# Optimization experiments

Hardware: AMD Instinct MI355X
Metric: run time of the kernel (lower is better)

The kernel has to match this reference:

```python
import jax, jax.numpy as jnp
import numpy as np

# dims: batch N, queries Q, frames F, patches-per-frame L, heads H, head_dim D
N, Q, F, L, H, D = 32, 64, 16, 196, 12, 64
E = H * D          # embed_dim = 768
K = F * L          # kv length = 3136


def setup_inputs() -> dict:
    key = jax.random.key(0)
    kq, kk, kv, km, kw1, kw2 = jax.random.split(key, 6)
    q = jax.random.normal(kq, (N, Q, E), dtype=jnp.float32)
    k = jax.random.normal(kk, (N, K, H, D), dtype=jnp.float32)
    v = jax.random.normal(kv, (N, K, H, D), dtype=jnp.float32)
    # frame-padding mask; guarantee >=1 valid patch per frame so the
    # per-frame softmax never sees an all -inf group (NaN otherwise)
    m = jax.random.bernoulli(km, 0.9, (N, K))
    m = m.reshape(N, F, L).at[:, :, 0].set(True).reshape(N, K)
    W_in = jax.random.normal(kw1, (E, E), dtype=jnp.float32) * 0.02   # in_proj (n_act=1)
    W_out = jax.random.normal(kw2, (E, E), dtype=jnp.float32) * 0.02  # out_proj
    return {"q": q, "k": k, "v": v, "m": m, "W_in": W_in, "W_out": W_out}


def reference(q, k, v, m, W_in, W_out):
    n, nq, e = q.shape
    h, d = H, e // H
    # in_proj (no bias) then split into heads; n_act == 1 so qs has one element
    qs = (q @ W_in.T).reshape(n, nq, h, d)
    # scaled QK affinity: [n, Q, K, h]
    aff = jnp.einsum('nqhc,nkhc->nqkh', qs * (d ** -0.5), k)
    # frame mask broadcast over queries and heads
    aff = jnp.where(m[:, None, :, None], aff, -jnp.inf)
    kn = aff.shape[2]
    # grouped softmax over patches within each frame (dim=-2 of the view)
    aff = jax.nn.softmax(aff.reshape(n, nq, F, kn // F, h), axis=-2)
    aff = aff.reshape(n, nq, kn, h)
    # mix with v and output projection
    mix = jnp.einsum('nqlh,nlhc->nqhc', aff, v)
    out = mix.reshape(n, nq, e) @ W_out.T
    # second return: stacked flattened qs, shape [n, n_act=1, Q, E]
    qs_out = qs.reshape(n, nq, e)[:, None]
    return out, qs_out
```

## Files before the change

### kernel.cpp

```cpp
#include <hip/hip_runtime.h>
#include <hip/hip_bf16.h>
#include <cfloat>

#define N_B 32
#define QN 64
#define FN 16
#define LP 196
#define HN 12
#define DH 64
#define EE 768
#define KLEN 3136
#define FPB 4
#define KROWS 208
#define VST 256
#define PST 232

typedef short s16x4 __attribute__((ext_vector_type(4)));
typedef __bf16 bf16x8 __attribute__((ext_vector_type(8)));
typedef float f32x4 __attribute__((ext_vector_type(4)));

__device__ __forceinline__ bf16x8 cvt8(f32x4 a, f32x4 b) {
    bf16x8 r;
    r[0] = (__bf16)a[0]; r[1] = (__bf16)a[1]; r[2] = (__bf16)a[2]; r[3] = (__bf16)a[3];
    r[4] = (__bf16)b[0]; r[5] = (__bf16)b[1]; r[6] = (__bf16)b[2]; r[7] = (__bf16)b[3];
    return r;
}
__device__ __forceinline__ unsigned short bfb(float x) {
    return __builtin_bit_cast(unsigned short, (__bf16)x);
}

__global__ __launch_bounds__(256) void gemm_mfma(const float* __restrict__ A,
                                                 const float* __restrict__ W,
                                                 float* __restrict__ C) {
    __shared__ unsigned short As[64 * 72];
    __shared__ unsigned short Ws[48 * 72];
    const int t = threadIdx.x;
    const int w = t >> 6, lane = t & 63, lr = lane & 15, lg = lane >> 4;
    const int m0 = blockIdx.x * 64;
    const int n0 = blockIdx.y * 48;

    f32x4 acc[3];
#pragma unroll
    for (int ct = 0; ct < 3; ++ct) acc[ct] = (f32x4){0.f, 0.f, 0.f, 0.f};

    for (int k0 = 0; k0 < EE; k0 += 32) {
        {
            int row = t >> 2, cb = t & 3;
            const float* src = A + (size_t)(m0 + row) * EE + k0 + cb * 8;
            f32x4 a = *(const f32x4*)src, b = *(const f32x4*)(src + 4);
            *(bf16x8*)&As[row * 72 + cb * 8] = cvt8(a, b);
        }
        if (t < 192) {
            int row = t >> 2, cb = t & 3;
            const float* src = W + (size_t)(n0 + row) * EE + k0 + cb * 8;
            f32x4 a = *(const f32x4*)src, b = *(const f32x4*)(src + 4);
            *(bf16x8*)&Ws[row * 72 + cb * 8] = cvt8(a, b);
        }
        __syncthreads();
        bf16x8 a = *(const bf16x8*)&As[(w * 16 + lr) * 72 + lg * 8];
#pragma unroll
        for (int ct = 0; ct < 3; ++ct) {
            bf16x8 b = *(const bf16x8*)&Ws[(ct * 16 + lr) * 72 + lg * 8];
            acc[ct] = __builtin_amdgcn_mfma_f32_16x16x32_bf16(a, b, acc[ct], 0, 0, 0);
        }
        __syncthreads();
    }
#pragma unroll
    for (int ct = 0; ct < 3; ++ct)
#pragma unroll
        for (int r = 0; r < 4; ++r)
            C[(size_t)(m0 + w * 16 + lg * 4 + r) * EE + n0 + ct * 16 + lr] = acc[ct][r];
}

__global__ __launch_bounds__(256) void zero_f32(float* __restrict__ p, int n4) {
    int i = blockIdx.x * 256 + threadIdx.x;
    if (i < n4) ((float4*)p)[i] = make_float4(0.f, 0.f, 0.f, 0.f);
}

__global__ __launch_bounds__(256, 2) void attn_mfma(const float* __restrict__ qs_g,
                                                    const float* __restrict__ k_g,
                                                    const float* __restrict__ v_g,
                                                    const int* __restrict__ m_g,
                                                    float* __restrict__ mix_g) {
    const int h = blockIdx.x, fg = blockIdx.y, n = blockIdx.z;

    __shared__ unsigned short KV_s[64 * VST];
    __shared__ unsigned short Pt_s[64 * PST];
    __shared__ float bias_s[224];
    __shared__ float linv_s[4][16];

    const int t = threadIdx.x;
    const int w = t >> 6, lane = t & 63, lr = lane & 15, lg = lane >> 4;

    {
        int qr = t >> 2, c0 = 208 + (t & 3) * 4;
        *(s16x4*)&Pt_s[qr * PST + c0] = (s16x4){0, 0, 0, 0};
    }
    bf16x8 qb0, qb1;
    {
        const float* qp = qs_g + ((size_t)n * QN + w * 16 + lr) * EE + h * DH + lg * 8;
        f32x4 a = *(const f32x4*)qp, b = *(const f32x4*)(qp + 4);
        f32x4 c = *(const f32x4*)(qp + 32), d = *(const f32x4*)(qp + 36);
#pragma unroll
        for (int i = 0; i < 4; ++i) { a[i] *= 0.125f; b[i] *= 0.125f; c[i] *= 0.125f; d[i] *= 0.125f; }
        qb0 = cvt8(a, b);
        qb1 = cvt8(c, d);
    }

    float mix[4][4];
#pragma unroll
    for (int dt = 0; dt < 4; ++dt)
#pragma unroll
        for (int r = 0; r < 4; ++r) mix[dt][r] = 0.f;

    for (int ff = 0; ff < FPB; ++ff) {
        const size_t kbase = (size_t)n * KLEN + (size_t)(fg * FPB + ff) * LP;

        __syncthreads();

#pragma unroll
        for (int u = 0; u < 7; ++u) {
            int unit = t + 256 * u;
            if (unit < KROWS * 8) {
                int p = unit >> 3, blk = unit & 7;
                f32x4 a = {0.f, 0.f, 0.f, 0.f}, b = {0.f, 0.f, 0.f, 0.f};
                if (p < LP) {
                    const float* src = k_g + ((kbase + p) * HN + h) * DH + blk * 8;
                    a = *(const f32x4*)src;
                    b = *(const f32x4*)(src + 4);
                }
                *(bf16x8*)&KV_s[p * 64 + ((blk ^ (p & 7)) << 3)] = cvt8(a, b);
            }
        }
        if (t < 224) {
            float bv = -1e30f;
            if (t < LP && m_g[kbase + t] != 0) bv = 0.f;
            bias_s[t] = bv;
        }
        __syncthreads();

        f32x4 sc[13];
#pragma unroll
        for (int tl = 0; tl < 13; ++tl) {
            int row = tl * 16 + lr;
            bf16x8 a0 = *(const bf16x8*)&KV_s[row * 64 + ((lg ^ (lr & 7)) << 3)];
            bf16x8 a1 = *(const bf16x8*)&KV_s[row * 64 + (((4 + lg) ^ (lr & 7)) << 3)];
            f32x4 z = {0.f, 0.f, 0.f, 0.f};
            z = __builtin_amdgcn_mfma_f32_16x16x32_bf16(a0, qb0, z, 0, 0, 0);
            sc[tl] = __builtin_amdgcn_mfma_f32_16x16x32_bf16(a1, qb1, z, 0, 0, 0);
        }

        f32x4 va[7], vb[7];
#pragma unroll
        for (int u = 0; u < 7; ++u) {
            int unit = t + 256 * u;
            int pp = unit >> 4, d4 = unit & 15;
            int p0 = pp * 2;
            va[u] = (f32x4){0.f, 0.f, 0.f, 0.f};
            vb[u] = (f32x4){0.f, 0.f, 0.f, 0.f};
            if (p0 < LP) {
                const float* vg = v_g + ((kbase + p0) * HN + h) * DH + d4 * 4;
                va[u] = *(const f32x4*)vg;
                if (p0 + 1 < LP) vb[u] = *(const f32x4*)(vg + (size_t)HN * DH);
            }
        }

        float mx = -FLT_MAX;
#pragma unroll
        for (int tl = 0; tl < 13; ++tl)
#pragma unroll
            for (int r = 0; r < 4; ++r) {
                float sv = sc[tl][r] + bias_s[tl * 16 + lg * 4 + r];
                sc[tl][r] = sv;
                mx = fmaxf(mx, sv);
            }
        mx = fmaxf(mx, __shfl_xor(mx, 16));
        mx = fmaxf(mx, __shfl_xor(mx, 32));
        float sum = 0.f;
#pragma unroll
        for (int tl = 0; tl < 13; ++tl)
#pragma unroll
            for (int r = 0; r < 4; ++r) {
                float e = __expf(sc[tl][r] - mx);
                sc[tl][r] = e;
                sum += e;
            }
        sum += __shfl_xor(sum, 16);
        sum += __shfl_xor(sum, 32);
        if (lane < 16) linv_s[w][lane] = 1.0f / sum;

#pragma unroll
        for (int tl = 0; tl < 13; ++tl) {
            s16x4 pb = {(short)bfb(sc[tl][0]), (short)bfb(sc[tl][1]),
                        (short)bfb(sc[tl][2]), (short)bfb(sc[tl][3])};
            *(s16x4*)&Pt_s[(w * 16 + lr) * PST + tl * 16 + lg * 4] = pb;
        }
        __syncthreads();

#pragma unroll
        for (int u = 0; u < 7; ++u) {
            int unit = t + 256 * u;
            int pp = unit >> 4, d4 = unit & 15;
            int p0 = pp * 2;
            int blk = p0 >> 3, sub = p0 & 7;
#pragma unroll
            for (int i = 0; i < 4; ++i) {
                int row = d4 * 4 + i;
                int g = (row + (row >> 2)) & 7;
                unsigned pk = (unsigned)bfb(va[u][i]) | ((unsigned)bfb(vb[u][i]) << 16);
                *(unsigned*)&KV_s[row * VST + (((blk ^ g) << 3) | sub)] = pk;
            }
        }
        __syncthreads();

        f32x4 pv[4];
#pragma unroll
        for (int dt = 0; dt < 4; ++dt) pv[dt] = (f32x4){0.f, 0.f, 0.f, 0.f};
#pragma unroll
        for (int ks = 0; ks < 7; ++ks) {
            bf16x8 a = *(const bf16x8*)&Pt_s[(w * 16 + lr) * PST + ks * 32 + lg * 8];
#pragma unroll
            for (int dt = 0; dt < 4; ++dt) {
                int row = dt * 16 + lr;
                int g = (row + (row >> 2)) & 7;
                bf16x8 b = *(const bf16x8*)&KV_s[row * VST + (((ks * 4 + lg) ^ g) << 3)];
                pv[dt] = __builtin_amdgcn_mfma_f32_16x16x32_bf16(a, b, pv[dt], 0, 0, 0);
            }
        }
        float li[4];
#pragma unroll
        for (int r = 0; r < 4; ++r) li[r] = linv_s[w][lg * 4 + r];
#pragma unroll
        for (int dt = 0; dt < 4; ++dt)
#pragma unroll
            for (int r = 0; r < 4; ++r) mix[dt][r] += pv[dt][r] * li[r];
    }

#pragma unroll
    for (int dt = 0; dt < 4; ++dt)
#pragma unroll
        for (int r = 0; r < 4; ++r)
            atomicAdd(mix_g + ((size_t)n * QN + w * 16 + lg * 4 + r) * EE + h * DH + dt * 16 + lr,
                      mix[dt][r]);
}

extern "C" void kernel_launch(void* const* d_in, const int* in_sizes, int n_in,
                              void* d_out, int out_size, void* d_ws, size_t ws_size,
                              hipStream_t stream) {
    const float* q  = (const float*)d_in[0];
    const float* k  = (const float*)d_in[1];
    const float* v  = (const float*)d_in[2];
    const int*   m  = (const int*)d_in[3];
    const float* Wi = (const float*)d_in[4];
    const float* Wo = (const float*)d_in[5];

    float* out = (float*)d_out;
    float* qs  = out + (size_t)N_B * QN * EE;
    float* mix = (float*)d_ws;

    const int mix_n4 = (N_B * QN * EE) / 4;
    dim3 ggrid((N_B * QN) / 64, EE / 48);
    gemm_mfma<<<ggrid, 256, 0, stream>>>(q, Wi, qs);
    zero_f32<<<(mix_n4 + 255) / 256, 256, 0, stream>>>(mix, mix_n4);
    attn_mfma<<<dim3(HN, FN / FPB, N_B), 256, 0, stream>>>(qs, k, v, m, mix);
    gemm_mfma<<<ggrid, 256, 0, stream>>>(mix, Wo, out);
}
```

Measured before the change: 221.6 us.

## Keep softmax probabilities in registers via lane shuffles, drop Pt LDS buffer

Removes the shared-memory staging of the bf16 probability matrix and the linv buffer. Probabilities are packed in registers and rearranged into the MFMA A-operand layout with cross-lane shuffles, and the 1/sum values are broadcast with shuffles. The smaller LDS footprint allows raising launch bounds to 4 blocks per CU, and FPB drops from 4 to 2, doubling the grid and the atomic adds. The V swizzle pattern changes, V loads move after the softmax (less register prefetch overlap), and the extra shuffles add VALU/LDS-permute work.

```diff
diff --git a/kernel.cpp b/kernel.cpp
--- a/kernel.cpp
+++ b/kernel.cpp
@@ -10,14 +10,14 @@
 #define DH 64
 #define EE 768
 #define KLEN 3136
-#define FPB 4
+#define FPB 2
 #define KROWS 208
 #define VST 256
-#define PST 232
 
 typedef short s16x4 __attribute__((ext_vector_type(4)));
 typedef __bf16 bf16x8 __attribute__((ext_vector_type(8)));
 typedef float f32x4 __attribute__((ext_vector_type(4)));
+typedef unsigned u32x4 __attribute__((ext_vector_type(4)));
 
 __device__ __forceinline__ bf16x8 cvt8(f32x4 a, f32x4 b) {
     bf16x8 r;
@@ -27,6 +27,9 @@
 }
 __device__ __forceinline__ unsigned short bfb(float x) {
     return __builtin_bit_cast(unsigned short, (__bf16)x);
+}
+__device__ __forceinline__ unsigned pkbf(float lo, float hi) {
+    return (unsigned)bfb(lo) | ((unsigned)bfb(hi) << 16);
 }
 
 __global__ __launch_bounds__(256) void gemm_mfma(const float* __restrict__ A,
@@ -77,25 +80,19 @@
     if (i < n4) ((float4*)p)[i] = make_float4(0.f, 0.f, 0.f, 0.f);
 }
 
-__global__ __launch_bounds__(256, 2) void attn_mfma(const float* __restrict__ qs_g,
+__global__ __launch_bounds__(256, 4) void attn_mfma(const float* __restrict__ qs_g,
                                                     const float* __restrict__ k_g,
                                                     const float* __restrict__ v_g,
                                                     const int* __restrict__ m_g,
                                                     float* __restrict__ mix_g) {
     const int h = blockIdx.x, fg = blockIdx.y, n = blockIdx.z;
 
-    __shared__ unsigned short KV_s[64 * VST];
-    __shared__ unsigned short Pt_s[64 * PST];
-    __shared__ float bias_s[224];
-    __shared__ float linv_s[4][16];
+    __shared__ __attribute__((aligned(16))) unsigned short KV_s[64 * VST];
+    __shared__ __attribute__((aligned(16))) float bias_s[224];
 
     const int t = threadIdx.x;
     const int w = t >> 6, lane = t & 63, lr = lane & 15, lg = lane >> 4;
 
-    {
-        int qr = t >> 2, c0 = 208 + (t & 3) * 4;
-        *(s16x4*)&Pt_s[qr * PST + c0] = (s16x4){0, 0, 0, 0};
-    }
     bf16x8 qb0, qb1;
     {
         const float* qp = qs_g + ((size_t)n * QN + w * 16 + lr) * EE + h * DH + lg * 8;
@@ -150,65 +147,58 @@
             sc[tl] = __builtin_amdgcn_mfma_f32_16x16x32_bf16(a1, qb1, z, 0, 0, 0);
         }
 
-        f32x4 va[7], vb[7];
+        float mx = -FLT_MAX;
+#pragma unroll
+        for (int tl = 0; tl < 13; ++tl) {
+            f32x4 bv = *(const f32x4*)&bias_s[tl * 16 + lg * 4];
+#pragma unroll
+            for (int r = 0; r < 4; ++r) {
+                float sv = sc[tl][r] + bv[r];
+                sc[tl][r] = sv;
+                mx = fmaxf(mx, sv);
+            }
+        }
+        mx = fmaxf(mx, __shfl_xor(mx, 16));
+        mx = fmaxf(mx, __shfl_xor(mx, 32));
+        float sum = 0.f;
+        unsigned pk[14][2];
+#pragma unroll
+        for (int tl = 0; tl < 13; ++tl) {
+            float e0 = __expf(sc[tl][0] - mx);
+            float e1 = __expf(sc[tl][1] - mx);
+            float e2 = __expf(sc[tl][2] - mx);
+            float e3 = __expf(sc[tl][3] - mx);
+            sum += (e0 + e1) + (e2 + e3);
+            pk[tl][0] = pkbf(e0, e1);
+            pk[tl][1] = pkbf(e2, e3);
+        }
+        pk[13][0] = 0u; pk[13][1] = 0u;
+        sum += __shfl_xor(sum, 16);
+        sum += __shfl_xor(sum, 32);
+        float inv = 1.0f / sum;
+        float li[4];
+#pragma unroll
+        for (int r = 0; r < 4; ++r) li[r] = __shfl(inv, lg * 4 + r);
+
+        __syncthreads();
+
 #pragma unroll
         for (int u = 0; u < 7; ++u) {
             int unit = t + 256 * u;
             int pp = unit >> 4, d4 = unit & 15;
             int p0 = pp * 2;
-            va[u] = (f32x4){0.f, 0.f, 0.f, 0.f};
-            vb[u] = (f32x4){0.f, 0.f, 0.f, 0.f};
+            f32x4 va = {0.f, 0.f, 0.f, 0.f}, vb = {0.f, 0.f, 0.f, 0.f};
             if (p0 < LP) {
                 const float* vg = v_g + ((kbase + p0) * HN + h) * DH + d4 * 4;
-                va[u] = *(const f32x4*)vg;
-                if (p0 + 1 < LP) vb[u] = *(const f32x4*)(vg + (size_t)HN * DH);
-            }
-        }
-
-        float mx = -FLT_MAX;
-#pragma unroll
-        for (int tl = 0; tl < 13; ++tl)
-#pragma unroll
-            for (int r = 0; r < 4; ++r) {
-                float sv = sc[tl][r] + bias_s[tl * 16 + lg * 4 + r];
-                sc[tl][r] = sv;
-                mx = fmaxf(mx, sv);
-            }
-        mx = fmaxf(mx, __shfl_xor(mx, 16));
-        mx = fmaxf(mx, __shfl_xor(mx, 32));
-        float sum = 0.f;
-#pragma unroll
-        for (int tl = 0; tl < 13; ++tl)
-#pragma unroll
-            for (int r = 0; r < 4; ++r) {
-                float e = __expf(sc[tl][r] - mx);
-                sc[tl][r] = e;
-                sum += e;
-            }
-        sum += __shfl_xor(sum, 16);
-        sum += __shfl_xor(sum, 32);
-        if (lane < 16) linv_s[w][lane] = 1.0f / sum;
-
-#pragma unroll
-        for (int tl = 0; tl < 13; ++tl) {
-            s16x4 pb = {(short)bfb(sc[tl][0]), (short)bfb(sc[tl][1]),
-                        (short)bfb(sc[tl][2]), (short)bfb(sc[tl][3])};
-            *(s16x4*)&Pt_s[(w * 16 + lr) * PST + tl * 16 + lg * 4] = pb;
-        }
-        __syncthreads();
-
-#pragma unroll
-        for (int u = 0; u < 7; ++u) {
-            int unit = t + 256 * u;
-            int pp = unit >> 4, d4 = unit & 15;
-            int p0 = pp * 2;
+                va = *(const f32x4*)vg;
+                vb = *(const f32x4*)(vg + (size_t)HN * DH);
+            }
             int blk = p0 >> 3, sub = p0 & 7;
 #pragma unroll
             for (int i = 0; i < 4; ++i) {
                 int row = d4 * 4 + i;
-                int g = (row + (row >> 2)) & 7;
-                unsigned pk = (unsigned)bfb(va[u][i]) | ((unsigned)bfb(vb[u][i]) << 16);
-                *(unsigned*)&KV_s[row * VST + (((blk ^ g) << 3) | sub)] = pk;
+                int g = (row + 2 * (row >> 2)) & 7;
+                *(unsigned*)&KV_s[row * VST + (((blk ^ g) << 3) | sub)] = pkbf(va[i], vb[i]);
             }
         }
         __syncthreads();
@@ -218,18 +208,28 @@
         for (int dt = 0; dt < 4; ++dt) pv[dt] = (f32x4){0.f, 0.f, 0.f, 0.f};
 #pragma unroll
         for (int ks = 0; ks < 7; ++ks) {
-            bf16x8 a = *(const bf16x8*)&Pt_s[(w * 16 + lr) * PST + ks * 32 + lg * 8];
+            unsigned a0 = pk[2 * ks][0],     a1 = pk[2 * ks][1];
+            unsigned b0 = pk[2 * ks + 1][0], b1 = pk[2 * ks + 1][1];
+            unsigned xA0 = __shfl_xor(a0, 16), xA1 = __shfl_xor(a1, 16);
+            unsigned yA0 = __shfl_xor(a0, 32), yA1 = __shfl_xor(a1, 32);
+            unsigned zA0 = __shfl_xor(a0, 48), zA1 = __shfl_xor(a1, 48);
+            unsigned xB0 = __shfl_xor(b0, 16), xB1 = __shfl_xor(b1, 16);
+            unsigned yB0 = __shfl_xor(b0, 32), yB1 = __shfl_xor(b1, 32);
+            unsigned zB0 = __shfl_xor(b0, 48), zB1 = __shfl_xor(b1, 48);
+            const bool lgb0 = (lg & 1) != 0, lgb1 = (lg >> 1) != 0;
+            unsigned s0 = lgb1 ? (lgb0 ? xB0 : yB0) : (lgb0 ? zA0 : a0);
+            unsigned s1 = lgb1 ? (lgb0 ? xB1 : yB1) : (lgb0 ? zA1 : a1);
+            unsigned s2 = lgb1 ? (lgb0 ? b0 : zB0) : (lgb0 ? yA0 : xA0);
+            unsigned s3 = lgb1 ? (lgb0 ? b1 : zB1) : (lgb0 ? yA1 : xA1);
+            bf16x8 pa = __builtin_bit_cast(bf16x8, (u32x4){s0, s1, s2, s3});
 #pragma unroll
             for (int dt = 0; dt < 4; ++dt) {
                 int row = dt * 16 + lr;
-                int g = (row + (row >> 2)) & 7;
-                bf16x8 b = *(const bf16x8*)&KV_s[row * VST + (((ks * 4 + lg) ^ g) << 3)];
-                pv[dt] = __builtin_amdgcn_mfma_f32_16x16x32_bf16(a, b, pv[dt], 0, 0, 0);
-            }
-        }
-        float li[4];
-#pragma unroll
-        for (int r = 0; r < 4; ++r) li[r] = linv_s[w][lg * 4 + r];
+                int g = (row + 2 * (row >> 2)) & 7;
+                bf16x8 b = *(const bf16x8*)&KV_s[row * VST + ((((ks * 4 + lg) ^ g)) << 3)];
+                pv[dt] = __builtin_amdgcn_mfma_f32_16x16x32_bf16(pa, b, pv[dt], 0, 0, 0);
+            }
+        }
 #pragma unroll
         for (int dt = 0; dt < 4; ++dt)
 #pragma unroll
```

Measured after the change: 317.5 us. 1.43x slower.
